# Performance work log

Hardware: AMD Instinct MI355X
Metric: run time of the kernel (lower is better)

Reference implementation:

```python
import jax, jax.numpy as jnp
import numpy as np

NS = 0.4      # neighborhood_size
GS = 8        # grid_size
RNN = 128     # rnn_size
EMB = 64      # embedding_size
NMIX = 20     # nmixtures
N = 1024      # num pedestrians


def setup_inputs() -> dict:
    key = jax.random.key(0)
    ks = jax.random.split(key, 14)
    s = 0.05
    return {
        "xoff": jax.random.normal(ks[0], (N, 2)) * s,
        "xabs": jax.random.uniform(ks[1], (N, 2)),
        "h0": jax.random.normal(ks[2], (1, N, RNN)) * 0.1,
        "c0": jax.random.normal(ks[3], (1, N, RNN)) * 0.1,
        "W_emb": jax.random.normal(ks[4], (EMB, 2)) * s,
        "b_emb": jax.random.normal(ks[5], (EMB,)) * s,
        "W_soc": jax.random.normal(ks[6], (EMB, GS * GS * RNN)) * s,
        "b_soc": jax.random.normal(ks[7], (EMB,)) * s,
        "W_ih": jax.random.normal(ks[8], (4 * RNN, 2 * EMB)) * s,
        "W_hh": jax.random.normal(ks[9], (4 * RNN, RNN)) * s,
        "b_ih": jax.random.normal(ks[10], (4 * RNN,)) * s,
        "b_hh": jax.random.normal(ks[11], (4 * RNN,)) * s,
        "W_out": jax.random.normal(ks[12], (6 * NMIX, RNN)) * s,
        "b_out": jax.random.normal(ks[13], (6 * NMIX,)) * s,
    }


def grid_mask(xabs, dtype):
    # Vectorized getGridMask: [N, N, GS*GS] one-hot neighbor binning.
    x, y = xabs[:, 0], xabs[:, 1]
    dx = x[None, :] - (x[:, None] - NS / 2)  # other_x - width_low, [N, N]
    dy = y[None, :] - (y[:, None] - NS / 2)
    cx = jnp.floor(dx / NS * GS).astype(jnp.int32)
    cy = jnp.floor(dy / NS * GS).astype(jnp.int32)
    n = x.shape[0]
    valid = ((dx >= 0) & (dx < NS) & (dy >= 0) & (dy < NS)
             & (cx >= 0) & (cx < GS) & (cy >= 0) & (cy < GS)
             & ~jnp.eye(n, dtype=bool))
    cell = jnp.clip(cx + cy * GS, 0, GS * GS - 1)
    return jax.nn.one_hot(cell, GS * GS, dtype=dtype) * valid[..., None].astype(dtype)


def reference(xoff, xabs, h0, c0, W_emb, b_emb, W_soc, b_soc,
              W_ih, W_hh, b_ih, b_hh, W_out, b_out):
    n = xabs.shape[0]
    # predict_distance=True -> embed offsets
    emb = jax.nn.relu(xoff @ W_emb.T + b_emb)                 # [N, 64]
    grid = grid_mask(xabs, emb.dtype)                          # [N, N, 64]
    h = h0[0]                                                  # [N, 128]
    # getSocialTensor: scatter neighbor hidden states into grid bins
    social = jnp.einsum('nmg,mh->ngh', grid, h).reshape(n, GS * GS * RNN)
    pool = jax.nn.relu(social @ W_soc.T + b_soc)               # [N, 64]
    xin = jnp.concatenate([emb, pool], axis=-1)                # [N, 128]
    # single-step LSTM, torch gate order i, f, g, o
    gates = xin @ W_ih.T + h @ W_hh.T + b_ih + b_hh            # [N, 512]
    i, f, g, o = jnp.split(gates, 4, axis=-1)
    c = jax.nn.sigmoid(f) * c0[0] + jax.nn.sigmoid(i) * jnp.tanh(g)
    hn = jax.nn.sigmoid(o) * jnp.tanh(c)
    out = hn @ W_out.T + b_out                                 # [N, 120]
    mu1, mu2, ls1, ls2, rho, pi_logits = jnp.split(out, 6, axis=1)
    return (mu1, mu2, ls1, ls2, rho, pi_logits)
```

## Files before the change

kernel.cpp:

```cpp
#include <hip/hip_runtime.h>
#include <hip/hip_bf16.h>

#define NN_ 1024

#define U_WGF  0
#define U_SHI  131072
#define U_ACTH 655360
#define U_P    917504
#define F_WOUT 2555904
#define F_HN   2572288
#define I_OFF  2703360
#define I_CNT  3751936

typedef __attribute__((ext_vector_type(8))) short short8;
typedef __attribute__((ext_vector_type(4))) float floatx4;

__device__ __forceinline__ float b2f_(unsigned short u) {
    return __uint_as_float(((unsigned)u) << 16);
}
__device__ __forceinline__ unsigned short f2bu(float f) {
    __hip_bfloat16 b = __float2bfloat16(f);
    return *(unsigned short*)&b;
}
__device__ __forceinline__ float ldin(const void* p, int i, int isbf) {
    return isbf ? b2f_(((const unsigned short*)p)[i]) : ((const float*)p)[i];
}
__device__ __forceinline__ int detect_bf16(const void* Wih, int tid) {
    unsigned wv = ((const unsigned*)Wih)[tid];
    unsigned e8 = (wv >> 7) & 0xFFu;
    return (__syncthreads_count((e8 >= 96u && e8 <= 134u) ? 1 : 0) > 128) ? 1 : 0;
}

__global__ __launch_bounds__(256) void prep_kernel(
        const void* __restrict__ xoff, const void* __restrict__ xabs,
        const void* __restrict__ h0,
        const void* __restrict__ Wsoc, const void* __restrict__ Wemb,
        const void* __restrict__ bemb, const void* __restrict__ Wih,
        const void* __restrict__ Whh,  const void* __restrict__ Wout,
        float* __restrict__ ws) {
    const int tid = threadIdx.x;
    const int bid = blockIdx.x;
    const int isbf = detect_bf16(Wih, tid);
    unsigned short* u = (unsigned short*)ws;

    if (bid < 424) {
        const int t0 = (bid * 256 + tid) * 8;
        unsigned short hv[8];
        if (t0 < 131072) {
            int jl = (t0 >> 3) & 15, q = (t0 >> 7) & 3, kb = (t0 >> 9) & 7, jt = t0 >> 12;
            int j = (jt & 3) * 128 + (jt >> 2) * 16 + jl;
            int k0 = kb * 32 + q * 8;
#pragma unroll
            for (int r = 0; r < 8; r++) {
                int k = k0 + r;
                float v = (k < 128) ? ldin(Wih, j * 128 + k, isbf)
                                    : ldin(Whh, j * 128 + (k - 128), isbf);
                hv[r] = f2bu(v);
            }
            *(short8*)(u + U_WGF + t0) = *(short8*)hv;
        } else if (t0 < 147456) {
            int t2 = t0 - 131072; int r = t2 >> 7, j0 = t2 & 127;
#pragma unroll
            for (int i = 0; i < 8; i++) {
                int j = j0 + i;
                ws[F_WOUT + t2 + i] = (j < 120) ? ldin(Wout, j * 128 + r, isbf) : 0.0f;
            }
        } else if (t0 < 671744) {
            int t2 = t0 - 147456;
            int e = (t2 >> 3) & 63, q = (t2 >> 9) & 3, j = (t2 >> 11) & 3, g = t2 >> 13;
            int src = e * 8192 + g * 128 + j * 32 + q * 8;
#pragma unroll
            for (int r = 0; r < 8; r++) hv[r] = f2bu(ldin(Wsoc, src + r, isbf));
            *(short8*)(u + U_SHI + t2) = *(short8*)hv;
        } else if (t0 < 802816) {
            int t2 = t0 - 671744; int n = t2 >> 7, k = t2 & 127;
#pragma unroll
            for (int i = 0; i < 8; i++) hv[i] = f2bu(ldin(h0, t2 + i, isbf));
            *(short8*)(u + U_ACTH + n * 256 + 128 + k) = *(short8*)hv;
        } else {
            int t2 = t0 - 802816; int n = t2 >> 6, e0 = t2 & 63;
            float x0 = ldin(xoff, 2 * n, isbf), x1 = ldin(xoff, 2 * n + 1, isbf);
#pragma unroll
            for (int i = 0; i < 8; i++) {
                int e = e0 + i;
                float v = fmaf(x0, ldin(Wemb, 2 * e, isbf),
                          fmaf(x1, ldin(Wemb, 2 * e + 1, isbf), ldin(bemb, e, isbf)));
                hv[i] = f2bu(fmaxf(v, 0.0f));
            }
            *(short8*)(u + U_ACTH + n * 256 + e0) = *(short8*)hv;
        }
    } else {
        __shared__ float xs_[2048];
        __shared__ int cnt_s[4];
        for (int i = tid; i < 2048; i += 256) xs_[i] = ldin(xabs, i, isbf);
        if (tid < 4) cnt_s[tid] = 0;
        __syncthreads();
        const int a = tid >> 6, t = tid & 63;
        const int n = (bid - 424) * 4 + a;
        unsigned* OFF = (unsigned*)ws + I_OFF + n * 1024;
        const float xsn = xs_[2 * n]     - 0.2f;
        const float ysn = xs_[2 * n + 1] - 0.2f;
        for (int i = t; i < NN_; i += 64) {
            float dx = xs_[2 * i]     - xsn;
            float dy = xs_[2 * i + 1] - ysn;
            int cx = (int)floorf(dx / 0.4f * 8.0f);
            int cy = (int)floorf(dy / 0.4f * 8.0f);
            bool valid = (dx >= 0.0f) && (dx < 0.4f) && (dy >= 0.0f) && (dy < 0.4f)
                      && (cx >= 0) && (cx < 8) && (cy >= 0) && (cy < 8) && (i != n);
            if (valid) {
                int pos = atomicAdd(&cnt_s[a], 1);
                OFF[pos] = (unsigned)(i * 4096 + ((cy * 8 + cx) << 6));
            }
        }
        __syncthreads();
        if (tid < 4) ((unsigned*)ws)[I_CNT + (bid - 424) * 4 + tid] = (unsigned)cnt_s[tid];
    }
}

__global__ __launch_bounds__(256) void pgemm_kernel(float* __restrict__ ws) {
    const unsigned short* u = (const unsigned short*)ws;
    const short* Ah  = (const short*)(u + U_ACTH);
    const short* Shi = (const short*)(u + U_SHI);
    unsigned short* P16 = (unsigned short*)ws + U_P;
    const int tid = threadIdx.x, lane = tid & 63, wv = tid >> 6;
    const int B_ = blockIdx.y * 64 + blockIdx.x;
    const int mtile = B_ & 63, rest = B_ >> 6;
    const int cg = rest >> 1, thalf = rest & 1;
    const int m = lane & 15, q = lane >> 4;
    const int g = cg * 4 + wv;
    const int abase = (mtile * 16 + m) * 256 + 128 + q * 8;
    short8 ah[4];
#pragma unroll
    for (int j = 0; j < 4; j++) ah[j] = *(const short8*)(Ah + abase + 32 * j);
    const int rowl = mtile * 16 + q * 4;
#pragma unroll
    for (int tt = 0; tt < 2; tt++) {
        const int t = thalf * 2 + tt;
        const int e = t * 16 + m;
        floatx4 c = {0.0f, 0.0f, 0.0f, 0.0f};
#pragma unroll
        for (int j = 0; j < 4; j++) {
            short8 bh = *(const short8*)(Shi + ((g * 4 + j) * 4 + q) * 512 + e * 8);
            c = __builtin_amdgcn_mfma_f32_16x16x32_bf16(ah[j], bh, c, 0, 0, 0);
        }
        const int n0 = cg * 256 + wv * 64 + t * 16;
#pragma unroll
        for (int r = 0; r < 4; r++)
            P16[(rowl + r) * 4096 + n0 + m] = f2bu(c[r]);
    }
}

__global__ __launch_bounds__(256) void pool_kernel(const void* __restrict__ b_soc,
                                                   const void* __restrict__ Wih_det,
                                                   float* __restrict__ ws) {
    __shared__ int off_s[1024];
    __shared__ float4 red4[16][16];
    const int tid = threadIdx.x;
    const int isbf = detect_bf16(Wih_det, tid);
    const int n = blockIdx.x;
    unsigned short* u = (unsigned short*)ws;
    const int cc = (int)((const unsigned*)ws)[I_CNT + n];
    {
        const unsigned* lst = (const unsigned*)ws + I_OFF + n * 1024;
        for (int j = tid; j < cc; j += 256) off_s[j] = (int)lst[j];
    }
    __syncthreads();
    {
        const unsigned short* P16 = (const unsigned short*)ws + U_P;
        const int strm = tid >> 4, e4 = tid & 15;
        float ax = 0.0f, ay = 0.0f, az = 0.0f, aw = 0.0f;
        for (int j = strm; j < cc; j += 16) {
            int o = off_s[j];
            ushort4 uu = *(const ushort4*)(P16 + o + 4 * e4);
            ax += b2f_(uu.x); ay += b2f_(uu.y); az += b2f_(uu.z); aw += b2f_(uu.w);
        }
        red4[strm][e4] = make_float4(ax, ay, az, aw);
    }
    __syncthreads();
    if (tid < 16) {
        float s[4] = {0.0f, 0.0f, 0.0f, 0.0f};
#pragma unroll
        for (int s16 = 0; s16 < 16; s16++) {
            float4 r = red4[s16][tid];
            s[0] += r.x; s[1] += r.y; s[2] += r.z; s[3] += r.w;
        }
        int e = 4 * tid;
#pragma unroll
        for (int i = 0; i < 4; i++) {
            float v = fmaxf(s[i] + ldin(b_soc, e + i, isbf), 0.0f);
            u[U_ACTH + n * 256 + 64 + e + i] = f2bu(v);
        }
    }
}

__global__ __launch_bounds__(256) void gates_kernel(const void* __restrict__ c0,
                                                    const void* __restrict__ b_ih,
                                                    const void* __restrict__ b_hh,
                                                    const void* __restrict__ Wih_det,
                                                    float* __restrict__ ws) {
    __shared__ float gl[16][68];
    const int tid = threadIdx.x;
    const int isbf = detect_bf16(Wih_det, tid);
    const unsigned short* u = (const unsigned short*)ws;
    const short* Ah = (const short*)(u + U_ACTH);
    const short* Wg = (const short*)(u + U_WGF);
    const int lane = tid & 63, wv = tid >> 6, m = lane & 15, q = lane >> 4;
    const int m0 = blockIdx.x * 16, y = blockIdx.y;
    const int jt = y * 4 + wv;
    floatx4 acc = {0.0f, 0.0f, 0.0f, 0.0f};
#pragma unroll
    for (int kb = 0; kb < 8; kb++) {
        short8 ah = *(const short8*)(Ah + (m0 + m) * 256 + kb * 32 + q * 8);
        short8 b  = *(const short8*)(Wg + (jt * 8 + kb) * 512 + q * 128 + m * 8);
        acc = __builtin_amdgcn_mfma_f32_16x16x32_bf16(ah, b, acc, 0, 0, 0);
    }
    const int jorig = wv * 128 + y * 16 + m;
    const float bias = ldin(b_ih, jorig, isbf) + ldin(b_hh, jorig, isbf);
#pragma unroll
    for (int r = 0; r < 4; r++)
        gl[q * 4 + r][wv * 16 + m] = acc[r] + bias;
    __syncthreads();
    {
        const int a = tid >> 4, rl = tid & 15;
        const int n = m0 + a, rg = y * 16 + rl;
        float iv = gl[a][rl],      fv = gl[a][16 + rl];
        float gv = gl[a][32 + rl], ov = gl[a][48 + rl];
        float si = 1.0f / (1.0f + expf(-iv));
        float sf = 1.0f / (1.0f + expf(-fv));
        float so = 1.0f / (1.0f + expf(-ov));
        float cc = sf * ldin(c0, n * 128 + rg, isbf) + si * tanhf(gv);
        ws[F_HN + n * 128 + rg] = so * tanhf(cc);
    }
}

__global__ __launch_bounds__(256) void pwout_kernel(const void* __restrict__ b_out,
                                                    const void* __restrict__ Wih_det,
                                                    const float* __restrict__ ws,
                                                    float* __restrict__ out) {
    __shared__ __align__(16) float hnl[2][128];
    const int tid = threadIdx.x;
    const int isbf = detect_bf16(Wih_det, tid);
    const int n0 = blockIdx.x * 2;
    const int half = tid >> 7, t2 = tid & 127;
    const int n = n0 + half;
    hnl[half][t2] = ws[F_HN + n * 128 + t2];
    __syncthreads();
    if (t2 < 120) {
        int j = t2;
        float acc = ldin(b_out, j, isbf);
        for (int r = 0; r < 128; r += 4) {
            float4 hq = *(const float4*)&hnl[half][r];
            acc = fmaf(hq.x, ws[F_WOUT + (r + 0) * 128 + j], acc);
            acc = fmaf(hq.y, ws[F_WOUT + (r + 1) * 128 + j], acc);
            acc = fmaf(hq.z, ws[F_WOUT + (r + 2) * 128 + j], acc);
            acc = fmaf(hq.w, ws[F_WOUT + (r + 3) * 128 + j], acc);
        }
        int ch = j / 20, wc = j - ch * 20;
        out[ch * 20480 + n * 20 + wc] = acc;
    }
}

extern "C" void kernel_launch(void* const* d_in, const int* in_sizes, int n_in,
                              void* d_out, int out_size, void* d_ws, size_t ws_size,
                              hipStream_t stream) {
    const void* xoff  = d_in[0];
    const void* xabs  = d_in[1];
    const void* h0    = d_in[2];
    const void* c0    = d_in[3];
    const void* W_emb = d_in[4];
    const void* b_emb = d_in[5];
    const void* W_soc = d_in[6];
    const void* b_soc = d_in[7];
    const void* W_ih  = d_in[8];
    const void* W_hh  = d_in[9];
    const void* b_ih  = d_in[10];
    const void* b_hh  = d_in[11];
    const void* W_out = d_in[12];
    const void* b_out = d_in[13];
    float* ws = (float*)d_ws;
    float* out = (float*)d_out;

    prep_kernel<<<680, 256, 0, stream>>>(xoff, xabs, h0, W_soc, W_emb, b_emb,
                                         W_ih, W_hh, W_out, ws);
    pgemm_kernel<<<dim3(64, 32), 256, 0, stream>>>(ws);
    pool_kernel<<<1024, 256, 0, stream>>>(b_soc, W_ih, ws);
    gates_kernel<<<dim3(64, 8), 256, 0, stream>>>(c0, b_ih, b_hh, W_ih, ws);
    pwout_kernel<<<512, 256, 0, stream>>>(b_out, W_ih, ws, out);
}
```

Before: 117.2 us.

## Fuse pool, LSTM gates, and output projection into one per-pedestrian tail kernel

Merges the pool, gates and output kernels into a single kernel with one block per pedestrian. The pooled activations, gate pre-activations and new hidden state stay in shared memory instead of going through global workspace. This saves two launches and the global round-trips. In exchange, each block runs the gate GEMM as a single-row MFMA with 15 of 16 A rows zeroed and reloads the full W_ih/W_hh fragment per pedestrian, which wastes matrix throughput and raises weight traffic.

```diff
diff --git a/kernel.cpp b/kernel.cpp
--- a/kernel.cpp
+++ b/kernel.cpp
@@ -8,7 +8,6 @@
 #define U_ACTH 655360
 #define U_P    917504
 #define F_WOUT 2555904
-#define F_HN   2572288
 #define I_OFF  2703360
 #define I_CNT  3751936
 
@@ -150,19 +149,28 @@
     }
 }
 
-__global__ __launch_bounds__(256) void pool_kernel(const void* __restrict__ b_soc,
+__global__ __launch_bounds__(256) void tail_kernel(const void* __restrict__ c0,
+                                                   const void* __restrict__ b_soc,
+                                                   const void* __restrict__ b_ih,
+                                                   const void* __restrict__ b_hh,
+                                                   const void* __restrict__ b_out,
                                                    const void* __restrict__ Wih_det,
-                                                   float* __restrict__ ws) {
+                                                   const float* __restrict__ ws,
+                                                   float* __restrict__ out) {
     __shared__ int off_s[1024];
     __shared__ float4 red4[16][16];
+    __shared__ __align__(16) unsigned short xin_b[256];
+    __shared__ float gate_s[512];
+    __shared__ __align__(16) float hn_s[128];
     const int tid = threadIdx.x;
     const int isbf = detect_bf16(Wih_det, tid);
+    const unsigned short* u = (const unsigned short*)ws;
     const int n = blockIdx.x;
-    unsigned short* u = (unsigned short*)ws;
     const int cc = (int)((const unsigned*)ws)[I_CNT + n];
     {
         const unsigned* lst = (const unsigned*)ws + I_OFF + n * 1024;
         for (int j = tid; j < cc; j += 256) off_s[j] = (int)lst[j];
+        if (tid < 64 || tid >= 128) xin_b[tid] = u[U_ACTH + n * 256 + tid];
     }
     __syncthreads();
     {
@@ -188,68 +196,51 @@
 #pragma unroll
         for (int i = 0; i < 4; i++) {
             float v = fmaxf(s[i] + ldin(b_soc, e + i, isbf), 0.0f);
-            u[U_ACTH + n * 256 + 64 + e + i] = f2bu(v);
-        }
-    }
-}
-
-__global__ __launch_bounds__(256) void gates_kernel(const void* __restrict__ c0,
-                                                    const void* __restrict__ b_ih,
-                                                    const void* __restrict__ b_hh,
-                                                    const void* __restrict__ Wih_det,
-                                                    float* __restrict__ ws) {
-    __shared__ float gl[16][68];
-    const int tid = threadIdx.x;
-    const int isbf = detect_bf16(Wih_det, tid);
-    const unsigned short* u = (const unsigned short*)ws;
-    const short* Ah = (const short*)(u + U_ACTH);
-    const short* Wg = (const short*)(u + U_WGF);
-    const int lane = tid & 63, wv = tid >> 6, m = lane & 15, q = lane >> 4;
-    const int m0 = blockIdx.x * 16, y = blockIdx.y;
-    const int jt = y * 4 + wv;
-    floatx4 acc = {0.0f, 0.0f, 0.0f, 0.0f};
-#pragma unroll
-    for (int kb = 0; kb < 8; kb++) {
-        short8 ah = *(const short8*)(Ah + (m0 + m) * 256 + kb * 32 + q * 8);
-        short8 b  = *(const short8*)(Wg + (jt * 8 + kb) * 512 + q * 128 + m * 8);
-        acc = __builtin_amdgcn_mfma_f32_16x16x32_bf16(ah, b, acc, 0, 0, 0);
-    }
-    const int jorig = wv * 128 + y * 16 + m;
-    const float bias = ldin(b_ih, jorig, isbf) + ldin(b_hh, jorig, isbf);
-#pragma unroll
-    for (int r = 0; r < 4; r++)
-        gl[q * 4 + r][wv * 16 + m] = acc[r] + bias;
+            xin_b[64 + e + i] = f2bu(v);
+        }
+    }
     __syncthreads();
     {
-        const int a = tid >> 4, rl = tid & 15;
-        const int n = m0 + a, rg = y * 16 + rl;
-        float iv = gl[a][rl],      fv = gl[a][16 + rl];
-        float gv = gl[a][32 + rl], ov = gl[a][48 + rl];
+        const int lane = tid & 63, wvv = tid >> 6, m = lane & 15, q = lane >> 4;
+        const short8 z8 = {0, 0, 0, 0, 0, 0, 0, 0};
+        short8 af[8];
+#pragma unroll
+        for (int kb = 0; kb < 8; kb++)
+            af[kb] = (m == 0) ? *(const short8*)(xin_b + kb * 32 + q * 8) : z8;
+        const short* Wg = (const short*)(u + U_WGF);
+#pragma unroll
+        for (int jt2 = 0; jt2 < 8; jt2++) {
+            const int jt = jt2 * 4 + wvv;
+            floatx4 acc = {0.0f, 0.0f, 0.0f, 0.0f};
+#pragma unroll
+            for (int kb = 0; kb < 8; kb++) {
+                short8 b = *(const short8*)(Wg + (jt * 8 + kb) * 512 + q * 128 + m * 8);
+                acc = __builtin_amdgcn_mfma_f32_16x16x32_bf16(af[kb], b, acc, 0, 0, 0);
+            }
+            if (q == 0) {
+                const int jorig = (jt & 3) * 128 + (jt >> 2) * 16 + m;
+                const float bias = ldin(b_ih, jorig, isbf) + ldin(b_hh, jorig, isbf);
+                gate_s[jorig] = acc[0] + bias;
+            }
+        }
+    }
+    __syncthreads();
+    if (tid < 128) {
+        const int r = tid;
+        float iv = gate_s[r],       fv = gate_s[128 + r];
+        float gv = gate_s[256 + r], ov = gate_s[384 + r];
         float si = 1.0f / (1.0f + expf(-iv));
         float sf = 1.0f / (1.0f + expf(-fv));
         float so = 1.0f / (1.0f + expf(-ov));
-        float cc = sf * ldin(c0, n * 128 + rg, isbf) + si * tanhf(gv);
-        ws[F_HN + n * 128 + rg] = so * tanhf(cc);
-    }
-}
-
-__global__ __launch_bounds__(256) void pwout_kernel(const void* __restrict__ b_out,
-                                                    const void* __restrict__ Wih_det,
-                                                    const float* __restrict__ ws,
-                                                    float* __restrict__ out) {
-    __shared__ __align__(16) float hnl[2][128];
-    const int tid = threadIdx.x;
-    const int isbf = detect_bf16(Wih_det, tid);
-    const int n0 = blockIdx.x * 2;
-    const int half = tid >> 7, t2 = tid & 127;
-    const int n = n0 + half;
-    hnl[half][t2] = ws[F_HN + n * 128 + t2];
-    __syncthreads();
-    if (t2 < 120) {
-        int j = t2;
+        float cv = sf * ldin(c0, n * 128 + r, isbf) + si * tanhf(gv);
+        hn_s[r] = so * tanhf(cv);
+    }
+    __syncthreads();
+    if (tid < 120) {
+        const int j = tid;
         float acc = ldin(b_out, j, isbf);
         for (int r = 0; r < 128; r += 4) {
-            float4 hq = *(const float4*)&hnl[half][r];
+            float4 hq = *(const float4*)&hn_s[r];
             acc = fmaf(hq.x, ws[F_WOUT + (r + 0) * 128 + j], acc);
             acc = fmaf(hq.y, ws[F_WOUT + (r + 1) * 128 + j], acc);
             acc = fmaf(hq.z, ws[F_WOUT + (r + 2) * 128 + j], acc);
@@ -283,7 +274,6 @@
     prep_kernel<<<680, 256, 0, stream>>>(xoff, xabs, h0, W_soc, W_emb, b_emb,
                                          W_ih, W_hh, W_out, ws);
     pgemm_kernel<<<dim3(64, 32), 256, 0, stream>>>(ws);
-    pool_kernel<<<1024, 256, 0, stream>>>(b_soc, W_ih, ws);
-    gates_kernel<<<dim3(64, 8), 256, 0, stream>>>(c0, b_ih, b_hh, W_ih, ws);
-    pwout_kernel<<<512, 256, 0, stream>>>(b_out, W_ih, ws, out);
-}
+    tail_kernel<<<1024, 256, 0, stream>>>(c0, b_soc, b_ih, b_hh, b_out,
+                                          W_ih, ws, out);
+}
```

After: 122.3 us. 4.3% more time.
